# Kernel optimization log

Measured on AMD Instinct MI355X. Metric: run time of the kernel, lower is better.

Reference implementation:

```python
import jax, jax.numpy as jnp
import numpy as np

B, T, C, HD = 16, 2048, 1024, 64


def setup_inputs() -> dict:
    key = jax.random.key(0)
    kx, kk, kq, kv = jax.random.split(key, 4)
    x = jax.random.normal(kx, (B, T, C), dtype=jnp.float32)
    Wk = jax.random.normal(kk, (C, HD), dtype=jnp.float32) * (C ** -0.5)
    Wq = jax.random.normal(kq, (C, HD), dtype=jnp.float32) * (C ** -0.5)
    Wv = jax.random.normal(kv, (C, HD), dtype=jnp.float32) * (C ** -0.5)
    return {"x": x, "Wk": Wk, "Wq": Wq, "Wv": Wv}


def reference(x, Wk, Wq, Wv):
    Bs, Ts, Cs = x.shape
    k = x @ Wk  # [B,T,HD]
    q = x @ Wq
    v = x @ Wv
    # Faithful to original: scores = key @ query^T, scaled by 1/sqrt(C) (embed dim!)
    scores = jnp.einsum('bth,bsh->bts', k, q) / jnp.sqrt(jnp.float32(Cs))
    causal = jnp.tril(jnp.ones((Ts, Ts), dtype=bool))  # tril[:T,:T]
    scores = jnp.where(causal, scores, -jnp.inf)
    weights = jax.nn.softmax(scores, axis=-1)  # [B,T,T]
    return jnp.einsum('bts,bsh->bth', weights, v)  # [B,T,HD]
```

## Files before the change

### kernel.cpp

```cpp
#include <hip/hip_runtime.h>
#include <hip/hip_bf16.h>

#define B_ 16
#define T_ 2048
#define C_ 1024
#define HD_ 64

typedef __attribute__((ext_vector_type(8))) short bf16x8;
typedef __attribute__((ext_vector_type(4))) float f32x4;

__device__ __forceinline__ unsigned short f2bf(float f) {
  return __builtin_bit_cast(unsigned short, __float2bfloat16(f));
}

__device__ __forceinline__ bf16x8 cvt8(float4 a, float4 b) {
  bf16x8 r;
  r[0] = (short)f2bf(a.x); r[1] = (short)f2bf(a.y);
  r[2] = (short)f2bf(a.z); r[3] = (short)f2bf(a.w);
  r[4] = (short)f2bf(b.x); r[5] = (short)f2bf(b.y);
  r[6] = (short)f2bf(b.z); r[7] = (short)f2bf(b.w);
  return r;
}

__global__ void wconv_kernel(const float* __restrict__ Wk, const float* __restrict__ Wq,
                             const float* __restrict__ Wv, unsigned short* __restrict__ wt2) {
  int o = blockIdx.x * 256 + threadIdx.x;
  if (o >= 3 * HD_ * C_) return;
  int r = o >> 10;
  int c = o & 1023;
  int s = c >> 3, e = c & 7;
  int lc = (((s & 0x78) | ((s ^ r) & 7)) << 3) | e;
  int m = r >> 6, d = r & 63;
  const float* W = (m == 0) ? Wk : (m == 1) ? Wq : Wv;
  float v = W[lc * HD_ + d];
  if (m == 0) v *= 0.03125f * 1.44269504088896f;
  wt2[o] = f2bf(v);
}

__global__ __launch_bounds__(256, 2) void qkv_kernel(const float* __restrict__ x,
                                                     const unsigned short* __restrict__ wt2,
                                                     unsigned short* __restrict__ kb,
                                                     unsigned short* __restrict__ qb,
                                                     unsigned short* __restrict__ vb) {
  __shared__ __align__(16) unsigned short wl[2 * 12288];

  const int tid = threadIdx.x;
  const int lane = tid & 63;
  const int w = tid >> 6;
  const int l15 = lane & 15;
  const int lh = lane >> 4;
  const int r0 = blockIdx.x * 64;
  const int sw = l15 & 7;
  const int c0 = (lh ^ sw) * 8;
  const int c1 = ((4 | lh) ^ sw) * 8;

  const float* xp = x + (size_t)(r0 + w * 16 + l15) * C_ + lh * 8;

  f32x4 acc[12];
#pragma unroll
  for (int i = 0; i < 12; ++i) acc[i] = {0.f, 0.f, 0.f, 0.f};

  float4 xr0[4], xr1[4], xr2[4];

#define STAGE(BUF, KK)                                                               \
  do {                                                                               \
    _Pragma("unroll")                                                                \
    for (int i_ = 0; i_ < 6; ++i_) {                                                 \
      const int gp_ = w * 6 + i_;                                                    \
      const int row_ = gp_ * 8 + (lane >> 3);                                        \
      const unsigned short* g_ = wt2 + row_ * 1024 + (KK) * 64 + (lane & 7) * 8;     \
      __builtin_amdgcn_global_load_lds(                                              \
          (const __attribute__((address_space(1))) void*)g_,                         \
          (__attribute__((address_space(3))) void*)&wl[(BUF) * 12288 + gp_ * 512],   \
          16, 0, 0);                                                                 \
    }                                                                                \
  } while (0)

#define XLOAD(XR, KK)                               \
  do {                                              \
    const float* p_ = xp + (KK) * 64;               \
    XR[0] = *(const float4*)(p_);                   \
    XR[1] = *(const float4*)(p_ + 4);               \
    XR[2] = *(const float4*)(p_ + 32);              \
    XR[3] = *(const float4*)(p_ + 36);              \
  } while (0)

#define COMPUTE(K, XR)                                                                   \
  do {                                                                                   \
    const unsigned short* wb = &wl[((K) & 1) * 12288];                                   \
    bf16x8 a0 = cvt8(XR[0], XR[1]);                                                      \
    bf16x8 a1 = cvt8(XR[2], XR[3]);                                                      \
    _Pragma("unroll")                                                                    \
    for (int cf = 0; cf < 12; ++cf) {                                                    \
      bf16x8 b0 = *(const bf16x8*)&wb[((cf >> 2) * 64 + (cf & 3) * 16 + l15) * 64 + c0]; \
      acc[cf] = __builtin_amdgcn_mfma_f32_16x16x32_bf16(a0, b0, acc[cf], 0, 0, 0);       \
    }                                                                                    \
    _Pragma("unroll")                                                                    \
    for (int cf = 0; cf < 12; ++cf) {                                                    \
      bf16x8 b1 = *(const bf16x8*)&wb[((cf >> 2) * 64 + (cf & 3) * 16 + l15) * 64 + c1]; \
      acc[cf] = __builtin_amdgcn_mfma_f32_16x16x32_bf16(a1, b1, acc[cf], 0, 0, 0);       \
    }                                                                                    \
  } while (0)

#define SB __builtin_amdgcn_sched_barrier(0)

#define ITER(K, XCUR, XPRE, VM)                                    \
  do {                                                             \
    if ((K) < 15) STAGE(((K) + 1) & 1, (K) + 1);                   \
    SB;                                                            \
    if ((K) < 14) XLOAD(XPRE, (K) + 2);                            \
    SB;                                                            \
    asm volatile("s_waitcnt vmcnt(" #VM ")" ::: "memory");         \
    SB;                                                            \
    __builtin_amdgcn_s_barrier();                                  \
    COMPUTE(K, XCUR);                                              \
    __builtin_amdgcn_s_barrier();                                  \
  } while (0)

  STAGE(0, 0);
  SB;
  XLOAD(xr0, 0);
  XLOAD(xr1, 1);
  SB;

  ITER(0, xr0, xr2, 14);
  ITER(1, xr1, xr0, 14);
  ITER(2, xr2, xr1, 14);
  ITER(3, xr0, xr2, 14);
  ITER(4, xr1, xr0, 14);
  ITER(5, xr2, xr1, 14);
  ITER(6, xr0, xr2, 14);
  ITER(7, xr1, xr0, 14);
  ITER(8, xr2, xr1, 14);
  ITER(9, xr0, xr2, 14);
  ITER(10, xr1, xr0, 14);
  ITER(11, xr2, xr1, 14);
  ITER(12, xr0, xr2, 14);
  ITER(13, xr1, xr0, 14);
  ITER(14, xr2, xr1, 10);
  ITER(15, xr0, xr2, 0);

#undef ITER
#undef COMPUTE
#undef XLOAD
#undef STAGE
#undef SB

#pragma unroll
  for (int cf = 0; cf < 4; ++cf) {
    int col = cf * 16 + l15;
#pragma unroll
    for (int r = 0; r < 4; ++r) {
      size_t row = (size_t)(r0 + w * 16 + lh * 4 + r);
      kb[row * HD_ + col] = f2bf(acc[cf][r]);
      qb[row * HD_ + col] = f2bf(acc[4 + cf][r]);
      vb[row * HD_ + col] = f2bf(acc[8 + cf][r]);
    }
  }
}

__global__ __launch_bounds__(256) void attn_kernel(const unsigned short* __restrict__ kb,
                                                   const unsigned short* __restrict__ qb,
                                                   const unsigned short* __restrict__ vb,
                                                   float* __restrict__ out) {
  __shared__ __align__(16) unsigned short q_lds[2][64 * 72];
  __shared__ __align__(16) unsigned short v_lds[2][64 * 72];
  __shared__ __align__(16) unsigned short p_lds[64 * 72];

  const int tid = threadIdx.x;
  const int lane = tid & 63;
  const int w = tid >> 6;
  const int bid = blockIdx.x;
  const int idx = bid >> 4;
  const int jt = (idx < 16) ? (31 - idx) : (idx - 16);
  const int b = bid & 15;
  const int t0 = jt * 64;
  const int l15 = lane & 15;
  const int lh = lane >> 4;
  const size_t base = (size_t)b * T_ * HD_;

  const int qrow = tid >> 3, qc8 = tid & 7;
  const int vss = tid & 63, vd0 = (tid >> 6) * 8;

  bf16x8 kf[2];
#pragma unroll
  for (int ks = 0; ks < 2; ++ks)
    kf[ks] = *reinterpret_cast<const bf16x8*>(
        &kb[base + (size_t)(t0 + w * 16 + l15) * HD_ + ks * 32 + lh * 8]);

  bf16x8 qr0, qr1, vr0, vr1;
  qr0 = *reinterpret_cast<const bf16x8*>(&qb[base + (size_t)qrow * HD_ + qc8 * 8]);
  qr1 = *reinterpret_cast<const bf16x8*>(&qb[base + (size_t)(qrow + 32) * HD_ + qc8 * 8]);
  vr0 = *reinterpret_cast<const bf16x8*>(&vb[base + (size_t)vss * HD_ + vd0]);
  vr1 = *reinterpret_cast<const bf16x8*>(&vb[base + (size_t)vss * HD_ + vd0 + 32]);

  f32x4 o[4];
#pragma unroll
  for (int i = 0; i < 4; ++i) o[i] = {0.f, 0.f, 0.f, 0.f};
  float mrun[4], lrun[4];
#pragma unroll
  for (int r = 0; r < 4; ++r) { mrun[r] = -1e30f; lrun[r] = 0.f; }

  for (int j = 0; j <= jt; ++j) {
    const int buf = j & 1;
    *reinterpret_cast<bf16x8*>(&q_lds[buf][qrow * 72 + qc8 * 8]) = qr0;
    *reinterpret_cast<bf16x8*>(&q_lds[buf][(qrow + 32) * 72 + qc8 * 8]) = qr1;
#pragma unroll
    for (int jj = 0; jj < 8; ++jj) v_lds[buf][(vd0 + jj) * 72 + vss] = (unsigned short)vr0[jj];
#pragma unroll
    for (int jj = 0; jj < 8; ++jj) v_lds[buf][(vd0 + 32 + jj) * 72 + vss] = (unsigned short)vr1[jj];
    __syncthreads();

    if (j < jt) {
      const size_t sb = base + (size_t)(j + 1) * 64 * HD_;
      qr0 = *reinterpret_cast<const bf16x8*>(&qb[sb + (size_t)qrow * HD_ + qc8 * 8]);
      qr1 = *reinterpret_cast<const bf16x8*>(&qb[sb + (size_t)(qrow + 32) * HD_ + qc8 * 8]);
      vr0 = *reinterpret_cast<const bf16x8*>(&vb[sb + (size_t)vss * HD_ + vd0]);
      vr1 = *reinterpret_cast<const bf16x8*>(&vb[sb + (size_t)vss * HD_ + vd0 + 32]);
    }
    __builtin_amdgcn_sched_barrier(0);

    f32x4 sf[4];
#pragma unroll
    for (int cf = 0; cf < 4; ++cf) sf[cf] = {0.f, 0.f, 0.f, 0.f};
    __builtin_amdgcn_s_setprio(1);
#pragma unroll
    for (int ks = 0; ks < 2; ++ks) {
#pragma unroll
      for (int cf = 0; cf < 4; ++cf) {
        bf16x8 bq = *reinterpret_cast<const bf16x8*>(&q_lds[buf][(cf * 16 + l15) * 72 + ks * 32 + lh * 8]);
        sf[cf] = __builtin_amdgcn_mfma_f32_16x16x32_bf16(kf[ks], bq, sf[cf], 0, 0, 0);
      }
    }
    __builtin_amdgcn_s_setprio(0);

    const bool diag = (j == jt);
    const int s0 = j * 64;
    float pv[4][4];
#pragma unroll
    for (int r = 0; r < 4; ++r) {
      const int tg = t0 + w * 16 + lh * 4 + r;
      float pm = -1e30f;
#pragma unroll
      for (int cf = 0; cf < 4; ++cf) {
        float v = sf[cf][r];
        if (diag && (s0 + cf * 16 + l15) > tg) v = -1e30f;
        pv[cf][r] = v;
        pm = fmaxf(pm, v);
      }
      pm = fmaxf(pm, __shfl_xor(pm, 1));
      pm = fmaxf(pm, __shfl_xor(pm, 2));
      pm = fmaxf(pm, __shfl_xor(pm, 4));
      pm = fmaxf(pm, __shfl_xor(pm, 8));
      float mn = fmaxf(mrun[r], pm);
      float scl = exp2f(mrun[r] - mn);
      mrun[r] = mn;
      float rs = 0.f;
#pragma unroll
      for (int cf = 0; cf < 4; ++cf) {
        float e = exp2f(pv[cf][r] - mn);
        pv[cf][r] = e;
        rs += e;
      }
      rs += __shfl_xor(rs, 1);
      rs += __shfl_xor(rs, 2);
      rs += __shfl_xor(rs, 4);
      rs += __shfl_xor(rs, 8);
      lrun[r] = lrun[r] * scl + rs;
#pragma unroll
      for (int df = 0; df < 4; ++df) o[df][r] *= scl;
    }
#pragma unroll
    for (int cf = 0; cf < 4; ++cf)
#pragma unroll
      for (int r = 0; r < 4; ++r)
        p_lds[(w * 16 + lh * 4 + r) * 72 + cf * 16 + l15] = f2bf(pv[cf][r]);

    __builtin_amdgcn_s_setprio(1);
#pragma unroll
    for (int ks = 0; ks < 2; ++ks) {
      bf16x8 pa = *reinterpret_cast<const bf16x8*>(&p_lds[(w * 16 + l15) * 72 + ks * 32 + lh * 8]);
#pragma unroll
      for (int df = 0; df < 4; ++df) {
        bf16x8 bv = *reinterpret_cast<const bf16x8*>(&v_lds[buf][(df * 16 + l15) * 72 + ks * 32 + lh * 8]);
        o[df] = __builtin_amdgcn_mfma_f32_16x16x32_bf16(pa, bv, o[df], 0, 0, 0);
      }
    }
    __builtin_amdgcn_s_setprio(0);
  }

#pragma unroll
  for (int r = 0; r < 4; ++r) {
    float inv = 1.f / lrun[r];
    int row = t0 + w * 16 + lh * 4 + r;
#pragma unroll
    for (int df = 0; df < 4; ++df)
      out[base + (size_t)row * HD_ + df * 16 + l15] = o[df][r] * inv;
  }
}

extern "C" void kernel_launch(void* const* d_in, const int* in_sizes, int n_in,
                              void* d_out, int out_size, void* d_ws, size_t ws_size,
                              hipStream_t stream) {
  const float* x  = (const float*)d_in[0];
  const float* Wk = (const float*)d_in[1];
  const float* Wq = (const float*)d_in[2];
  const float* Wv = (const float*)d_in[3];
  float* out = (float*)d_out;

  char* ws = (char*)d_ws;
  unsigned short* wt2 = (unsigned short*)ws;
  unsigned short* kb = (unsigned short*)(ws + 524288);
  unsigned short* qb = (unsigned short*)(ws + 524288 + 4 * 1024 * 1024);
  unsigned short* vb = (unsigned short*)(ws + 524288 + 8 * 1024 * 1024);

  hipLaunchKernelGGL(wconv_kernel, dim3(768), dim3(256), 0, stream, Wk, Wq, Wv, wt2);
  hipLaunchKernelGGL(qkv_kernel, dim3(512), dim3(256), 0, stream, x, wt2, kb, qb, vb);
  hipLaunchKernelGGL(attn_kernel, dim3(512), dim3(256), 0, stream, kb, qb, vb, out);
}
```

Measured before the change: 90.15 us.

## Pre-pack weights in MFMA fragment order and load directly from global, dropping LDS

The weight conversion kernel now writes the bf16 weights in the exact per-lane MFMA B-fragment order, so the QKV projection kernel loads each fragment with one 16-byte global load per lane. This replaces the LDS double-buffer, the global_load_lds staging and the block-wide barriers with a register ring of three fragment groups prefetched two ahead. The intent is to remove barrier stalls and LDS traffic. In exchange, every wave re-reads the weights through L2/L1 instead of sharing them in LDS, and it uses more registers.

```diff
diff --git a/kernel.cpp b/kernel.cpp
--- a/kernel.cpp
+++ b/kernel.cpp
@@ -23,128 +23,90 @@
 }
 
 __global__ void wconv_kernel(const float* __restrict__ Wk, const float* __restrict__ Wq,
-                             const float* __restrict__ Wv, unsigned short* __restrict__ wt2) {
+                             const float* __restrict__ Wv, unsigned short* __restrict__ wfrag) {
   int o = blockIdx.x * 256 + threadIdx.x;
-  if (o >= 3 * HD_ * C_) return;
-  int r = o >> 10;
-  int c = o & 1023;
-  int s = c >> 3, e = c & 7;
-  int lc = (((s & 0x78) | ((s ^ r) & 7)) << 3) | e;
-  int m = r >> 6, d = r & 63;
+  if (o >= 16 * 24 * 64 * 8) return;
+  int e = o & 7;
+  int lane = (o >> 3) & 63;
+  int t = o >> 9;
+  int kk = t / 24;
+  int f = t % 24;
+  int ks = f / 12;
+  int cf = f % 12;
+  int l15 = lane & 15, lh = lane >> 4;
+  int m = cf >> 2;
+  int d = (cf & 3) * 16 + l15;
+  int k = kk * 64 + ks * 32 + lh * 8 + e;
   const float* W = (m == 0) ? Wk : (m == 1) ? Wq : Wv;
-  float v = W[lc * HD_ + d];
+  float v = W[k * HD_ + d];
   if (m == 0) v *= 0.03125f * 1.44269504088896f;
-  wt2[o] = f2bf(v);
+  wfrag[o] = f2bf(v);
 }
 
 __global__ __launch_bounds__(256, 2) void qkv_kernel(const float* __restrict__ x,
-                                                     const unsigned short* __restrict__ wt2,
+                                                     const unsigned short* __restrict__ wfrag,
                                                      unsigned short* __restrict__ kb,
                                                      unsigned short* __restrict__ qb,
                                                      unsigned short* __restrict__ vb) {
-  __shared__ __align__(16) unsigned short wl[2 * 12288];
-
   const int tid = threadIdx.x;
   const int lane = tid & 63;
   const int w = tid >> 6;
   const int l15 = lane & 15;
   const int lh = lane >> 4;
   const int r0 = blockIdx.x * 64;
-  const int sw = l15 & 7;
-  const int c0 = (lh ^ sw) * 8;
-  const int c1 = ((4 | lh) ^ sw) * 8;
 
   const float* xp = x + (size_t)(r0 + w * 16 + l15) * C_ + lh * 8;
+  const unsigned short* wp = wfrag + lane * 8;
 
   f32x4 acc[12];
 #pragma unroll
   for (int i = 0; i < 12; ++i) acc[i] = {0.f, 0.f, 0.f, 0.f};
 
-  float4 xr0[4], xr1[4], xr2[4];
-
-#define STAGE(BUF, KK)                                                               \
-  do {                                                                               \
-    _Pragma("unroll")                                                                \
-    for (int i_ = 0; i_ < 6; ++i_) {                                                 \
-      const int gp_ = w * 6 + i_;                                                    \
-      const int row_ = gp_ * 8 + (lane >> 3);                                        \
-      const unsigned short* g_ = wt2 + row_ * 1024 + (KK) * 64 + (lane & 7) * 8;     \
-      __builtin_amdgcn_global_load_lds(                                              \
-          (const __attribute__((address_space(1))) void*)g_,                         \
-          (__attribute__((address_space(3))) void*)&wl[(BUF) * 12288 + gp_ * 512],   \
-          16, 0, 0);                                                                 \
-    }                                                                                \
+  float4 xr[2][4];
+  bf16x8 wg[3][4];
+
+#define WLOAD(SLOT, GQ)                                                        \
+  do {                                                                         \
+    _Pragma("unroll")                                                          \
+    for (int i_ = 0; i_ < 4; ++i_)                                             \
+      wg[SLOT][i_] = *(const bf16x8*)(wp + ((GQ) * 4 + i_) * 512);             \
   } while (0)
 
-#define XLOAD(XR, KK)                               \
-  do {                                              \
-    const float* p_ = xp + (KK) * 64;               \
-    XR[0] = *(const float4*)(p_);                   \
-    XR[1] = *(const float4*)(p_ + 4);               \
-    XR[2] = *(const float4*)(p_ + 32);              \
-    XR[3] = *(const float4*)(p_ + 36);              \
+#define XLOAD(SLOT, KK)                                 \
+  do {                                                  \
+    const float* p_ = xp + (KK) * 64;                   \
+    xr[SLOT][0] = *(const float4*)(p_);                 \
+    xr[SLOT][1] = *(const float4*)(p_ + 4);             \
+    xr[SLOT][2] = *(const float4*)(p_ + 32);            \
+    xr[SLOT][3] = *(const float4*)(p_ + 36);            \
   } while (0)
 
-#define COMPUTE(K, XR)                                                                   \
-  do {                                                                                   \
-    const unsigned short* wb = &wl[((K) & 1) * 12288];                                   \
-    bf16x8 a0 = cvt8(XR[0], XR[1]);                                                      \
-    bf16x8 a1 = cvt8(XR[2], XR[3]);                                                      \
-    _Pragma("unroll")                                                                    \
-    for (int cf = 0; cf < 12; ++cf) {                                                    \
-      bf16x8 b0 = *(const bf16x8*)&wb[((cf >> 2) * 64 + (cf & 3) * 16 + l15) * 64 + c0]; \
-      acc[cf] = __builtin_amdgcn_mfma_f32_16x16x32_bf16(a0, b0, acc[cf], 0, 0, 0);       \
-    }                                                                                    \
-    _Pragma("unroll")                                                                    \
-    for (int cf = 0; cf < 12; ++cf) {                                                    \
-      bf16x8 b1 = *(const bf16x8*)&wb[((cf >> 2) * 64 + (cf & 3) * 16 + l15) * 64 + c1]; \
-      acc[cf] = __builtin_amdgcn_mfma_f32_16x16x32_bf16(a1, b1, acc[cf], 0, 0, 0);       \
-    }                                                                                    \
-  } while (0)
-
-#define SB __builtin_amdgcn_sched_barrier(0)
-
-#define ITER(K, XCUR, XPRE, VM)                                    \
-  do {                                                             \
-    if ((K) < 15) STAGE(((K) + 1) & 1, (K) + 1);                   \
-    SB;                                                            \
-    if ((K) < 14) XLOAD(XPRE, (K) + 2);                            \
-    SB;                                                            \
-    asm volatile("s_waitcnt vmcnt(" #VM ")" ::: "memory");         \
-    SB;                                                            \
-    __builtin_amdgcn_s_barrier();                                  \
-    COMPUTE(K, XCUR);                                              \
-    __builtin_amdgcn_s_barrier();                                  \
-  } while (0)
-
-  STAGE(0, 0);
-  SB;
-  XLOAD(xr0, 0);
-  XLOAD(xr1, 1);
-  SB;
-
-  ITER(0, xr0, xr2, 14);
-  ITER(1, xr1, xr0, 14);
-  ITER(2, xr2, xr1, 14);
-  ITER(3, xr0, xr2, 14);
-  ITER(4, xr1, xr0, 14);
-  ITER(5, xr2, xr1, 14);
-  ITER(6, xr0, xr2, 14);
-  ITER(7, xr1, xr0, 14);
-  ITER(8, xr2, xr1, 14);
-  ITER(9, xr0, xr2, 14);
-  ITER(10, xr1, xr0, 14);
-  ITER(11, xr2, xr1, 14);
-  ITER(12, xr0, xr2, 14);
-  ITER(13, xr1, xr0, 14);
-  ITER(14, xr2, xr1, 10);
-  ITER(15, xr0, xr2, 0);
-
-#undef ITER
-#undef COMPUTE
+  XLOAD(0, 0);
+  WLOAD(0, 0);
+  WLOAD(1, 1);
+
+#pragma unroll
+  for (int kk = 0; kk < 16; ++kk) {
+    if (kk < 15) XLOAD((kk + 1) & 1, kk + 1);
+    bf16x8 a0 = cvt8(xr[kk & 1][0], xr[kk & 1][1]);
+    bf16x8 a1 = cvt8(xr[kk & 1][2], xr[kk & 1][3]);
+#pragma unroll
+    for (int g = 0; g < 6; ++g) {
+      const int GQ = kk * 6 + g;
+      if (GQ + 2 <= 95) WLOAD((GQ + 2) % 3, GQ + 2);
+#pragma unroll
+      for (int i = 0; i < 4; ++i) {
+        const int f = g * 4 + i;
+        const int cf = f % 12;
+        if (f < 12)
+          acc[cf] = __builtin_amdgcn_mfma_f32_16x16x32_bf16(a0, wg[GQ % 3][i], acc[cf], 0, 0, 0);
+        else
+          acc[cf] = __builtin_amdgcn_mfma_f32_16x16x32_bf16(a1, wg[GQ % 3][i], acc[cf], 0, 0, 0);
+      }
+    }
+  }
+#undef WLOAD
 #undef XLOAD
-#undef STAGE
-#undef SB
 
 #pragma unroll
   for (int cf = 0; cf < 4; ++cf) {
@@ -309,12 +271,12 @@
   float* out = (float*)d_out;
 
   char* ws = (char*)d_ws;
-  unsigned short* wt2 = (unsigned short*)ws;
+  unsigned short* wfrag = (unsigned short*)ws;
   unsigned short* kb = (unsigned short*)(ws + 524288);
   unsigned short* qb = (unsigned short*)(ws + 524288 + 4 * 1024 * 1024);
   unsigned short* vb = (unsigned short*)(ws + 524288 + 8 * 1024 * 1024);
 
-  hipLaunchKernelGGL(wconv_kernel, dim3(768), dim3(256), 0, stream, Wk, Wq, Wv, wt2);
-  hipLaunchKernelGGL(qkv_kernel, dim3(512), dim3(256), 0, stream, x, wt2, kb, qb, vb);
+  hipLaunchKernelGGL(wconv_kernel, dim3(768), dim3(256), 0, stream, Wk, Wq, Wv, wfrag);
+  hipLaunchKernelGGL(qkv_kernel, dim3(512), dim3(256), 0, stream, x, wfrag, kb, qb, vb);
   hipLaunchKernelGGL(attn_kernel, dim3(512), dim3(256), 0, stream, kb, qb, vb, out);
 }
```

After: 128.5 us. 1.42x slower.

## Deepen QKV projection weight pipeline to six LDS stages with larger blocks

Applied to the files above, without the earlier changes.

The QKV projection kernel now uses 512-thread blocks covering 128 rows, which halves the grid and shares each staged weight tile across twice as many rows. Weights are pre-laid out per K-chunk so the LDS copy is a contiguous async load. A six-deep ring of LDS buffers with loads issued five chunks ahead replaces the double buffer and drops the trailing barrier per iteration. The aim is to hide weight-load latency and cut global weight traffic. The cost is 144KB of LDS per block, which may limit occupancy, and the halved grid of 256 blocks may leave compute units underused.

```diff
diff --git a/kernel.cpp b/kernel.cpp
--- a/kernel.cpp
+++ b/kernel.cpp
@@ -13,48 +13,39 @@
   return __builtin_bit_cast(unsigned short, __float2bfloat16(f));
 }
 
-__device__ __forceinline__ bf16x8 cvt8(float4 a, float4 b) {
-  bf16x8 r;
-  r[0] = (short)f2bf(a.x); r[1] = (short)f2bf(a.y);
-  r[2] = (short)f2bf(a.z); r[3] = (short)f2bf(a.w);
-  r[4] = (short)f2bf(b.x); r[5] = (short)f2bf(b.y);
-  r[6] = (short)f2bf(b.z); r[7] = (short)f2bf(b.w);
-  return r;
-}
-
 __global__ void wconv_kernel(const float* __restrict__ Wk, const float* __restrict__ Wq,
-                             const float* __restrict__ Wv, unsigned short* __restrict__ wt2) {
+                             const float* __restrict__ Wv, unsigned short* __restrict__ w3) {
   int o = blockIdx.x * 256 + threadIdx.x;
-  if (o >= 3 * HD_ * C_) return;
-  int r = o >> 10;
-  int c = o & 1023;
-  int s = c >> 3, e = c & 7;
-  int lc = (((s & 0x78) | ((s ^ r) & 7)) << 3) | e;
-  int m = r >> 6, d = r & 63;
+  if (o >= 16 * 12288) return;
+  int kk = o / 12288;
+  int n = o - kk * 12288;
+  int row = n >> 6;
+  int c = (n >> 3) & 7;
+  int e = n & 7;
+  int k = kk * 64 + (((c ^ (row & 7)) << 3) | e);
+  int m = row >> 6, d = row & 63;
   const float* W = (m == 0) ? Wk : (m == 1) ? Wq : Wv;
-  float v = W[lc * HD_ + d];
+  float v = W[k * HD_ + d];
   if (m == 0) v *= 0.03125f * 1.44269504088896f;
-  wt2[o] = f2bf(v);
-}
-
-__global__ __launch_bounds__(256, 2) void qkv_kernel(const float* __restrict__ x,
-                                                     const unsigned short* __restrict__ wt2,
+  w3[o] = f2bf(v);
+}
+
+__global__ __launch_bounds__(512, 2) void qkv_kernel(const float* __restrict__ x,
+                                                     const unsigned short* __restrict__ w3,
                                                      unsigned short* __restrict__ kb,
                                                      unsigned short* __restrict__ qb,
                                                      unsigned short* __restrict__ vb) {
-  __shared__ __align__(16) unsigned short wl[2 * 12288];
+  __shared__ __align__(16) unsigned short wl[6 * 12288];
 
   const int tid = threadIdx.x;
   const int lane = tid & 63;
   const int w = tid >> 6;
-  const int l15 = lane & 15;
-  const int lh = lane >> 4;
-  const int r0 = blockIdx.x * 64;
-  const int sw = l15 & 7;
-  const int c0 = (lh ^ sw) * 8;
-  const int c1 = ((4 | lh) ^ sw) * 8;
+  const int l15 = lane & 15, lh = lane >> 4;
+  const int r0 = blockIdx.x * 128;
 
   const float* xp = x + (size_t)(r0 + w * 16 + l15) * C_ + lh * 8;
+  const int fb0 = l15 * 64 + ((lh ^ (l15 & 7)) << 3);
+  const int fb1 = l15 * 64 + (((4 | lh) ^ (l15 & 7)) << 3);
 
   f32x4 acc[12];
 #pragma unroll
@@ -62,65 +53,65 @@
 
   float4 xr0[4], xr1[4], xr2[4];
 
-#define STAGE(BUF, KK)                                                               \
+#define STAGE(KK)                                                                    \
   do {                                                                               \
     _Pragma("unroll")                                                                \
-    for (int i_ = 0; i_ < 6; ++i_) {                                                 \
-      const int gp_ = w * 6 + i_;                                                    \
-      const int row_ = gp_ * 8 + (lane >> 3);                                        \
-      const unsigned short* g_ = wt2 + row_ * 1024 + (KK) * 64 + (lane & 7) * 8;     \
+    for (int i_ = 0; i_ < 3; ++i_) {                                                 \
+      const int eo_ = ((w * 3 + i_) << 9) + lane * 8;     \
       __builtin_amdgcn_global_load_lds(                                              \
-          (const __attribute__((address_space(1))) void*)g_,                         \
-          (__attribute__((address_space(3))) void*)&wl[(BUF) * 12288 + gp_ * 512],   \
+          (const __attribute__((address_space(1))) void*)(w3 + (KK) * 12288 + eo_),  \
+          (__attribute__((address_space(3))) void*)&wl[((KK) % 6) * 12288 + eo_],    \
           16, 0, 0);                                                                 \
     }                                                                                \
   } while (0)
 
-#define XLOAD(XR, KK)                               \
-  do {                                              \
-    const float* p_ = xp + (KK) * 64;               \
-    XR[0] = *(const float4*)(p_);                   \
-    XR[1] = *(const float4*)(p_ + 4);               \
-    XR[2] = *(const float4*)(p_ + 32);              \
-    XR[3] = *(const float4*)(p_ + 36);              \
+#define XLOAD(XR, KK) do { const float* p_ = xp + (KK) * 64;                   \
+    XR[0] = *(const float4*)(p_);      XR[1] = *(const float4*)(p_ + 4);       \
+    XR[2] = *(const float4*)(p_ + 32); XR[3] = *(const float4*)(p_ + 36); } while (0)
+
+#define COMPUTE(S, XR)                                                               \
+  do {                                                                               \
+    const unsigned short* wb_ = &wl[((S) % 6) * 12288];                              \
+    bf16x8 a0 = cvt8_(XR[0], XR[1]);                                                 \
+    bf16x8 a1 = cvt8_(XR[2], XR[3]);                                                 \
+    _Pragma("unroll")                                                                \
+    for (int f_ = 0; f_ < 12; ++f_) {                                                \
+      bf16x8 b0 = *(const bf16x8*)&wb_[f_ * 1024 + fb0];                             \
+      acc[f_] = __builtin_amdgcn_mfma_f32_16x16x32_bf16(a0, b0, acc[f_], 0, 0, 0);   \
+      bf16x8 b1 = *(const bf16x8*)&wb_[f_ * 1024 + fb1];                             \
+      acc[f_] = __builtin_amdgcn_mfma_f32_16x16x32_bf16(a1, b1, acc[f_], 0, 0, 0);   \
+    }                                                                                \
   } while (0)
 
-#define COMPUTE(K, XR)                                                                   \
-  do {                                                                                   \
-    const unsigned short* wb = &wl[((K) & 1) * 12288];                                   \
-    bf16x8 a0 = cvt8(XR[0], XR[1]);                                                      \
-    bf16x8 a1 = cvt8(XR[2], XR[3]);                                                      \
-    _Pragma("unroll")                                                                    \
-    for (int cf = 0; cf < 12; ++cf) {                                                    \
-      bf16x8 b0 = *(const bf16x8*)&wb[((cf >> 2) * 64 + (cf & 3) * 16 + l15) * 64 + c0]; \
-      acc[cf] = __builtin_amdgcn_mfma_f32_16x16x32_bf16(a0, b0, acc[cf], 0, 0, 0);       \
-    }                                                                                    \
-    _Pragma("unroll")                                                                    \
-    for (int cf = 0; cf < 12; ++cf) {                                                    \
-      bf16x8 b1 = *(const bf16x8*)&wb[((cf >> 2) * 64 + (cf & 3) * 16 + l15) * 64 + c1]; \
-      acc[cf] = __builtin_amdgcn_mfma_f32_16x16x32_bf16(a1, b1, acc[cf], 0, 0, 0);       \
-    }                                                                                    \
-  } while (0)
-
 #define SB __builtin_amdgcn_sched_barrier(0)
 
-#define ITER(K, XCUR, XPRE, VM)                                    \
+#define cvt8_(A, Bv) ({ bf16x8 r_;                                              \
+    r_[0] = (short)f2bf((A).x); r_[1] = (short)f2bf((A).y);                     \
+    r_[2] = (short)f2bf((A).z); r_[3] = (short)f2bf((A).w);                     \
+    r_[4] = (short)f2bf((Bv).x); r_[5] = (short)f2bf((Bv).y);                   \
+    r_[6] = (short)f2bf((Bv).z); r_[7] = (short)f2bf((Bv).w); r_; })
+
+#define ITER(S, XCUR, XPRE, VM)                                    \
   do {                                                             \
-    if ((K) < 15) STAGE(((K) + 1) & 1, (K) + 1);                   \
-    SB;                                                            \
-    if ((K) < 14) XLOAD(XPRE, (K) + 2);                            \
+    if ((S) <= 13) { XLOAD(XPRE, (S) + 2); }                       \
     SB;                                                            \
     asm volatile("s_waitcnt vmcnt(" #VM ")" ::: "memory");         \
     SB;                                                            \
     __builtin_amdgcn_s_barrier();                                  \
-    COMPUTE(K, XCUR);                                              \
-    __builtin_amdgcn_s_barrier();                                  \
+    if ((S) <= 10) STAGE((S) + 5);                                 \
+    SB;                                                            \
+    COMPUTE(S, XCUR);                                              \
   } while (0)
 
-  STAGE(0, 0);
+  STAGE(0); STAGE(1); STAGE(2);
   SB;
   XLOAD(xr0, 0);
+  SB;
+  STAGE(3);
+  SB;
   XLOAD(xr1, 1);
+  SB;
+  STAGE(4);
   SB;
 
   ITER(0, xr0, xr2, 14);
@@ -135,16 +126,17 @@
   ITER(9, xr0, xr2, 14);
   ITER(10, xr1, xr0, 14);
   ITER(11, xr2, xr1, 14);
-  ITER(12, xr0, xr2, 14);
-  ITER(13, xr1, xr0, 14);
-  ITER(14, xr2, xr1, 10);
+  ITER(12, xr0, xr2, 11);
+  ITER(13, xr1, xr0, 8);
+  ITER(14, xr2, xr1, 4);
   ITER(15, xr0, xr2, 0);
 
 #undef ITER
+#undef cvt8_
+#undef SB
 #undef COMPUTE
 #undef XLOAD
 #undef STAGE
-#undef SB
 
 #pragma unroll
   for (int cf = 0; cf < 4; ++cf) {
@@ -309,12 +301,12 @@
   float* out = (float*)d_out;
 
   char* ws = (char*)d_ws;
-  unsigned short* wt2 = (unsigned short*)ws;
+  unsigned short* w3 = (unsigned short*)ws;
   unsigned short* kb = (unsigned short*)(ws + 524288);
   unsigned short* qb = (unsigned short*)(ws + 524288 + 4 * 1024 * 1024);
   unsigned short* vb = (unsigned short*)(ws + 524288 + 8 * 1024 * 1024);
 
-  hipLaunchKernelGGL(wconv_kernel, dim3(768), dim3(256), 0, stream, Wk, Wq, Wv, wt2);
-  hipLaunchKernelGGL(qkv_kernel, dim3(512), dim3(256), 0, stream, x, wt2, kb, qb, vb);
+  hipLaunchKernelGGL(wconv_kernel, dim3(768), dim3(256), 0, stream, Wk, Wq, Wv, w3);
+  hipLaunchKernelGGL(qkv_kernel, dim3(256), dim3(512), 0, stream, x, w3, kb, qb, vb);
   hipLaunchKernelGGL(attn_kernel, dim3(512), dim3(256), 0, stream, kb, qb, vb, out);
 }
```

Result: slower. 94.24 us (+4.5%).
